# Kernel tuning notes

Hardware: AMD Instinct MI355X
Metric: run time of the kernel (lower is better)

The kernel has to match this reference:

```python
import jax, jax.numpy as jnp
import numpy as np

INPUT_DIM = 4096
BOTTLENECK = 32768
A = 2
K = 0.05
# eval-mode sparsity count: max(1, int(bottleneck * a * k))
K_COUNT = max(1, int(BOTTLENECK * A * K))  # 3276


def setup_inputs() -> dict:
    key = jax.random.key(0)
    kx, kw = jax.random.split(key)
    x = jax.random.normal(kx, (4096, INPUT_DIM), dtype=jnp.float32)
    # encoder weight [bottleneck, input_dim], like nn.Linear(input_dim, bottleneck)
    W = jax.random.normal(kw, (BOTTLENECK, INPUT_DIM), dtype=jnp.float32) * (1.0 / np.sqrt(INPUT_DIM))
    b_enc = jnp.zeros((BOTTLENECK,), dtype=jnp.float32)
    b_dec = jnp.zeros((INPUT_DIM,), dtype=jnp.float32)
    return {"x": x, "W": W, "b_enc": b_enc, "b_dec": b_dec, "epoch": 0}


def reference(x, W, b_enc, b_dec, epoch):
    # encode: z1 = x @ W^T + b_enc  -> [B, bottleneck]
    z1 = jnp.einsum("bi,hi->bh", x, W) + b_enc
    # eval-mode k-winner-take-all mask over dim 1
    _, topk_idx = jax.lax.top_k(z1, K_COUNT)  # [B, K_COUNT]
    rows = jnp.arange(z1.shape[0])[:, None]
    mask = jnp.zeros_like(z1).at[rows, topk_idx].set(1.0)
    a1 = z1 * mask
    # tied-weight decode: z2 = a1 @ W + b_dec -> [B, input_dim]
    z2 = jnp.einsum("bh,hi->bi", a1, W) + b_dec
    return z2
```

## Files before the change

kernel.cpp:

```cpp
#include <hip/hip_runtime.h>
#include <hip/hip_bf16.h>
#include <stdint.h>


#define DIM      4096
#define BATCH    4096
#define NROWS_W  32768
#define KCNT     3276
#define DELTA    0.0066f
#define ROWCAP   256
#define HCAP     64

typedef __bf16 bf16x8 __attribute__((ext_vector_type(8)));
typedef __bf16 bf16x4 __attribute__((ext_vector_type(4)));
typedef float  f32x4  __attribute__((ext_vector_type(4)));

__device__ __forceinline__ void gload_lds16(const void* g, void* l) {
  __builtin_amdgcn_global_load_lds(
      (const __attribute__((address_space(1))) void*)g,
      (__attribute__((address_space(3))) void*)l, 16, 0, 0);
}

__global__ void k_split(const float* __restrict__ s, __bf16* __restrict__ hi,
                        __bf16* __restrict__ lo, int n4) {
  int i = blockIdx.x * 256 + threadIdx.x;
  const int stride = gridDim.x * 256;
  for (; i < n4; i += stride) {
    f32x4 v = ((const f32x4*)s)[i];
    bf16x4 h, l;
#pragma unroll
    for (int j = 0; j < 4; ++j) {
      __bf16 hb = (__bf16)v[j];
      h[j] = hb;
      l[j] = (__bf16)(v[j] - (float)hb);
    }
    ((bf16x4*)hi)[i] = h;
    ((bf16x4*)lo)[i] = l;
  }
}

__global__ void k_splitw(const float* __restrict__ W, __bf16* __restrict__ Wh,
                         __bf16* __restrict__ Wt) {
  __shared__ __bf16 t[64][65];
  const int c0 = blockIdx.x * 64, r0 = blockIdx.y * 64;
  const int tx = threadIdx.x, ty = threadIdx.y;
  for (int rr = ty; rr < 64; rr += 8) {
    const float w = W[(long)(r0 + rr) * DIM + c0 + tx];
    const __bf16 h = (__bf16)w;
    Wh[(long)(r0 + rr) * DIM + c0 + tx] = h;
    t[rr][tx] = h;
  }
  __syncthreads();
  for (int cc = ty; cc < 64; cc += 8)
    Wt[(long)(c0 + cc) * NROWS_W + r0 + tx] = t[tx][cc];
}

__global__ __launch_bounds__(256, 2)
void k_gemm(const __bf16* __restrict__ A, const __bf16* __restrict__ B,
            const float* __restrict__ bias, float* __restrict__ C,
            int M, int N, int Kt) {
  constexpr int BM = 128, BN = 128, BK = 64;
  __shared__ __align__(16) __bf16 sA[BM * BK];
  __shared__ __align__(16) __bf16 sB[BN * BK];

  const int tid = threadIdx.x;
  const int nbn = N / BN;
  int bm, bn;
  if ((M / BM) % 16 == 0 && nbn % 32 == 0) {
    const int nsbn = nbn / 32;
    const int g = blockIdx.x >> 9, r = blockIdx.x & 511;
    bm = (g / nsbn) * 16 + (r >> 5);
    bn = (g % nsbn) * 32 + (r & 31);
  } else {
    bm = blockIdx.x / nbn;
    bn = blockIdx.x % nbn;
  }
  const int m0 = bm * BM, n0 = bn * BN;
  const int lane = tid & 63, wid = tid >> 6;
  const int wm = wid >> 1, wn = wid & 1;
  const int lr = lane & 15, lk = lane >> 4;
  const int swz = (lr & 7) << 4;

  f32x4 acc[4][4] = {};

  for (int k0 = 0; k0 < Kt; k0 += BK) {
#pragma unroll
    for (int r = 0; r < 4; ++r) {
      const int o = (r * 256 + tid) * 16;
      const int row = o >> 7;
      const int colb = (o & 127) ^ ((row & 7) << 4);
      const long gA = ((long)(m0 + row) * Kt + k0) * 2 + colb;
      const long gB = ((long)(n0 + row) * Kt + k0) * 2 + colb;
      gload_lds16((const char*)A + gA, (char*)sA + o);
      gload_lds16((const char*)B + gB, (char*)sB + o);
    }
    __syncthreads();

#pragma unroll
    for (int kk = 0; kk < 2; ++kk) {
      bf16x8 va[4], vb[4];
      const int kbase = (kk * 64 + lk * 16) ^ swz;
#pragma unroll
      for (int m = 0; m < 4; ++m) {
        const int row = wm * 64 + m * 16 + lr;
        va[m] = *(const bf16x8*)((const char*)sA + row * 128 + kbase);
      }
#pragma unroll
      for (int n = 0; n < 4; ++n) {
        const int row = wn * 64 + n * 16 + lr;
        vb[n] = *(const bf16x8*)((const char*)sB + row * 128 + kbase);
      }
#pragma unroll
      for (int m = 0; m < 4; ++m)
#pragma unroll
        for (int n = 0; n < 4; ++n)
          acc[m][n] = __builtin_amdgcn_mfma_f32_16x16x32_bf16(va[m], vb[n], acc[m][n], 0, 0, 0);
    }
    __syncthreads();
  }

#pragma unroll
  for (int n = 0; n < 4; ++n) {
    const int col = n0 + wn * 64 + n * 16 + lr;
    const float bv = bias[col];
#pragma unroll
    for (int m = 0; m < 4; ++m) {
      const int r0r = m0 + wm * 64 + m * 16 + lk * 4;
#pragma unroll
      for (int j = 0; j < 4; ++j)
        C[(long)(r0r + j) * N + col] = acc[m][n][j] + bv;
    }
  }
}

__device__ __forceinline__ unsigned f2o(float f) {
  unsigned b = __float_as_uint(f);
  return ((int)b < 0) ? ~b : (b | 0x80000000u);
}
__device__ __forceinline__ float o2f(unsigned u) {
  unsigned b = (u & 0x80000000u) ? (u & 0x7FFFFFFFu) : ~u;
  return __uint_as_float(b);
}

__global__ __launch_bounds__(256)
void k_topk3(const float* __restrict__ z1, float* __restrict__ thr,
             unsigned* __restrict__ rowlist, unsigned* __restrict__ rowcnt,
             unsigned* __restrict__ c1, unsigned* __restrict__ bucket,
             unsigned* __restrict__ bcnt, int kwant) {
  __shared__ unsigned hist[4096];
  __shared__ unsigned cand[3584];
  __shared__ unsigned s_n, s_bin, s_rem, s_wt[4], s_cnt, s_above;
  const int tid = threadIdx.x;
  const int b = blockIdx.x;
  const f32x4* zv = (const f32x4*)(z1 + (long)b * NROWS_W);
  constexpr int NV = NROWS_W / 4;

#pragma unroll
  for (int j = 0; j < 16; ++j) hist[tid + j * 256] = 0;
  if (tid == 0) { s_n = 0; s_cnt = 0; s_above = 0; }
  __syncthreads();
  for (int i = tid; i < NV; i += 256) {
    f32x4 v = zv[i];
#pragma unroll
    for (int j = 0; j < 4; ++j) atomicAdd(&hist[f2o(v[j]) >> 20], 1u);
  }
  __syncthreads();
  unsigned p = 0;
#pragma unroll
  for (int j = 0; j < 16; ++j) p += hist[tid * 16 + j];
  unsigned sfx = p;
  const int lane = tid & 63, w = tid >> 6;
#pragma unroll
  for (int off = 1; off < 64; off <<= 1) {
    unsigned o = __shfl_down(sfx, off);
    sfx += (lane + off < 64) ? o : 0u;
  }
  if (lane == 0) s_wt[w] = sfx;
  __syncthreads();
  unsigned above_waves = 0;
  for (int ww = w + 1; ww < 4; ++ww) above_waves += s_wt[ww];
  const unsigned incl = sfx + above_waves;
  const int cnt = __syncthreads_count(incl >= (unsigned)kwant);
  const int tstar = cnt - 1;
  if (tid == tstar) {
    unsigned cum = incl - p;
    int bsel = tid * 16;
    for (int j = 15; j >= 0; --j) {
      const unsigned h = hist[tid * 16 + j];
      if (cum + h >= (unsigned)kwant) { bsel = tid * 16 + j; break; }
      cum += h;
    }
    s_bin = (unsigned)bsel;
    s_rem = (unsigned)kwant - cum;
  }
  __syncthreads();
  const unsigned binsel = s_bin;
  unsigned rem = s_rem;

  for (int i = tid; i < NV; i += 256) {
    f32x4 v = zv[i];
#pragma unroll
    for (int j = 0; j < 4; ++j) {
      const unsigned u = f2o(v[j]);
      if ((u >> 20) == binsel) {
        const unsigned jj = atomicAdd(&s_n, 1u);
        if (jj < 3584u) cand[jj] = u & 0xFFFFFu;
      }
    }
  }
  __syncthreads();
  const int n = (s_n < 3584u) ? (int)s_n : 3584;
  unsigned pfx = 0;
#pragma unroll
  for (int pass = 0; pass < 3; ++pass) {
    const int shift = (pass == 0) ? 12 : (pass == 1) ? 4 : 0;
    const int nb = (pass == 2) ? 16 : 256;
    if (tid < 256) hist[tid] = 0;
    __syncthreads();
    for (int i = tid; i < n; i += 256) {
      const unsigned v = cand[i];
      const bool m = (pass == 0) ? true
                     : (pass == 1) ? ((v >> 12) == (pfx >> 12))
                                   : ((v >> 4) == (pfx >> 4));
      if (m) atomicAdd(&hist[(v >> shift) & (nb - 1)], 1u);
    }
    __syncthreads();
    if (tid == 0) {
      unsigned cum = 0;
      int d = nb - 1;
      for (; d > 0; --d) {
        if (cum + hist[d] >= rem) break;
        cum += hist[d];
      }
      s_bin = (unsigned)d;
      s_rem = rem - cum;
    }
    __syncthreads();
    pfx |= (s_bin << shift);
    rem = s_rem;
    __syncthreads();
  }
  const float t = o2f((binsel << 20) | pfx);
  if (tid == 0) thr[b] = t;
  __syncthreads();

  const float hi = t + DELTA, lo = t - DELTA;
  unsigned my_above = 0;
  for (int i = tid; i < NV; i += 256) {
    f32x4 v = zv[i];
#pragma unroll
    for (int j = 0; j < 4; ++j) {
      const float vv = v[j];
      my_above += (vv > hi) ? 1u : 0u;
      if (vv >= lo && vv <= hi) {
        const unsigned idx = (unsigned)(i * 4 + j);
        const unsigned jj = atomicAdd(&s_cnt, 1u);
        if (jj < ROWCAP) {
          rowlist[(long)b * ROWCAP + jj] = idx;
          const unsigned pq = atomicAdd(&bcnt[idx], 1u);
          if (pq < HCAP) bucket[(long)idx * HCAP + pq] = ((unsigned)b << 9) | jj;
        }
      }
    }
  }
  atomicAdd(&s_above, my_above);
  __syncthreads();
  if (tid == 0) {
    rowcnt[b] = (s_cnt < ROWCAP) ? s_cnt : ROWCAP;
    c1[b] = s_above;
  }
}

__global__ void k_zero(f32x4* __restrict__ p, int nvec) {
  int i = blockIdx.x * 256 + threadIdx.x;
  const int stride = gridDim.x * 256;
  f32x4 z = {0.f, 0.f, 0.f, 0.f};
  for (; i < nvec; i += stride) p[i] = z;
}

__global__ void k_recompute(const float* __restrict__ W, const __bf16* __restrict__ xh,
                            const __bf16* __restrict__ xl,
                            const unsigned* __restrict__ bucket,
                            const unsigned* __restrict__ bcnt,
                            float* __restrict__ exact) {
  const int h = blockIdx.x;
  unsigned n = bcnt[h];
  if (n > HCAP) n = HCAP;
  if (n == 0) return;
  __shared__ float wrec[DIM];
  const long wb = (long)h * DIM;
  for (int i = threadIdx.x; i < DIM / 4; i += 256)
    ((f32x4*)wrec)[i] = ((const f32x4*)(W + wb))[i];
  __syncthreads();
  const int w = threadIdx.x >> 6, lane = threadIdx.x & 63;
  for (unsigned e = w; e < n; e += 4) {
    const unsigned ent = bucket[(long)h * HCAP + e];
    const int b = ent >> 9, j = ent & 511;
    const bf16x8* ph = (const bf16x8*)(xh + (long)b * DIM);
    const bf16x8* pl = (const bf16x8*)(xl + (long)b * DIM);
    float s = 0.f;
#pragma unroll
    for (int c = 0; c < 8; ++c) {
      const int i8 = c * 64 + lane;
      bf16x8 vh = ph[i8], vl = pl[i8];
      const float* wr = &wrec[i8 * 8];
#pragma unroll
      for (int q = 0; q < 8; ++q) s += ((float)vh[q] + (float)vl[q]) * wr[q];
    }
#pragma unroll
    for (int m = 32; m; m >>= 1) s += __shfl_xor(s, m);
    if (lane == 0) exact[(long)b * ROWCAP + j] = s;
  }
}

__global__ void k_select(const float* __restrict__ exact, const unsigned* __restrict__ rowlist,
                         const unsigned* __restrict__ rowcnt, const unsigned* __restrict__ c1,
                         unsigned* __restrict__ bitmap) {
  const int b = blockIdx.x;
  const int n = (int)rowcnt[b];
  const int need = KCNT - (int)c1[b];
  __shared__ float vals[ROWCAP];
  const int j = threadIdx.x;
  vals[j] = (j < n) ? exact[(long)b * ROWCAP + j] : -1e30f;
  __syncthreads();
  if (j < n) {
    const float vj = vals[j];
    int rank = 0;
    for (int i = 0; i < n; ++i) {
      const float vi = vals[i];
      rank += (vi > vj || (vi == vj && i < j)) ? 1 : 0;
    }
    if (rank < need) {
      const unsigned h = rowlist[(long)b * ROWCAP + j];
      atomicOr(&bitmap[b * (NROWS_W / 32) + (h >> 5)], 1u << (h & 31));
    }
  }
}

__global__ void k_mask(const float* __restrict__ z1, const float* __restrict__ thr,
                       const unsigned* __restrict__ bitmap, __bf16* __restrict__ a1,
                       int n4, int ncols4) {
  int i = blockIdx.x * 256 + threadIdx.x;
  const int stride = gridDim.x * 256;
  for (; i < n4; i += stride) {
    f32x4 v = ((const f32x4*)z1)[i];
    const int row = i / ncols4;
    const int h0 = (i - row * ncols4) * 4;
    const float t = thr[row];
    const float hi = t + DELTA, lo = t - DELTA;
    const unsigned wbits = bitmap[row * (NROWS_W / 32) + (h0 >> 5)];
    bf16x4 o;
#pragma unroll
    for (int j = 0; j < 4; ++j) {
      const float vv = v[j];
      const bool sel = (vv > hi) || (vv >= lo && ((wbits >> ((h0 + j) & 31)) & 1u));
      o[j] = sel ? (__bf16)vv : (__bf16)0.0f;
    }
    ((bf16x4*)a1)[i] = o;
  }
}

extern "C" void kernel_launch(void* const* d_in, const int* in_sizes, int n_in,
                              void* d_out, int out_size, void* d_ws, size_t ws_size,
                              hipStream_t stream) {
  const float* x     = (const float*)d_in[0];
  const float* W     = (const float*)d_in[1];
  const float* b_enc = (const float*)d_in[2];
  const float* b_dec = (const float*)d_in[3];
  float* out = (float*)d_out;

  const long NW = (long)NROWS_W * DIM;
  const long NX = (long)BATCH * DIM;
  const long NZ = (long)BATCH * NROWS_W;

  char* ws = (char*)d_ws;
  __bf16* Wh = (__bf16*)ws;
  __bf16* Wt = Wh + NW;
  __bf16* xh = Wt + NW;
  __bf16* xl = xh + NX;
  float*  z1 = (float*)(xl + NX);
  float*  thr = z1 + NZ;
  char*   sc = (char*)(thr + BATCH);
  unsigned* rowcnt  = (unsigned*)sc;
  unsigned* c1      = (unsigned*)(sc + 16384);
  unsigned* bcnt    = (unsigned*)(sc + 32768);
  unsigned* bitmap  = (unsigned*)(sc + 163840);
  float*    exact   = (float*)(sc + 16941056);
  unsigned* rowlist = (unsigned*)(sc + 21135360);
  unsigned* bucket  = (unsigned*)(sc + 25329664);
  const long ZERO_OFF = 32768, ZERO_BYTES = 21069824;
  __bf16* a1 = Wh;

  const size_t needed = (size_t)(6 * NW + 4 * NX) + (size_t)4 * NZ + 4 * BATCH;
  if (ws_size < needed) return;

  k_splitw<<<dim3(DIM / 64, NROWS_W / 64), dim3(64, 8), 0, stream>>>(W, Wh, Wt);
  k_split<<<2048, 256, 0, stream>>>(x, xh, xl, (int)(NX / 4));

  k_gemm<<<(BATCH / 128) * (NROWS_W / 128), 256, 0, stream>>>(
      xh, Wh, b_enc, z1, BATCH, NROWS_W, DIM);

  k_zero<<<1024, 256, 0, stream>>>((f32x4*)(sc + ZERO_OFF), (int)(ZERO_BYTES / 16));
  k_topk3<<<BATCH, 256, 0, stream>>>(z1, thr, rowlist, rowcnt, c1, bucket, bcnt, KCNT);
  k_recompute<<<NROWS_W, 256, 0, stream>>>(W, xh, xl, bucket, bcnt, exact);
  k_select<<<BATCH, ROWCAP, 0, stream>>>(exact, rowlist, rowcnt, c1, bitmap);
  k_mask<<<2048, 256, 0, stream>>>(z1, thr, bitmap, a1, (int)(NZ / 4), NROWS_W / 4);

  k_gemm<<<(BATCH / 128) * (DIM / 128), 256, 0, stream>>>(
      a1, Wt, b_dec, out, BATCH, DIM, NROWS_W);
}
```

Baseline: 3.635 ms.

## Fuse mask into top-k, gather band candidates in LDS, drop x lo split

Result: faster. 3.553 ms (-2.3%).

```diff
diff --git a/kernel.cpp b/kernel.cpp
--- a/kernel.cpp
+++ b/kernel.cpp
@@ -10,6 +10,7 @@
 #define DELTA    0.0066f
 #define ROWCAP   256
 #define HCAP     64
+#define CANDCAP  3584
 
 typedef __bf16 bf16x8 __attribute__((ext_vector_type(8)));
 typedef __bf16 bf16x4 __attribute__((ext_vector_type(4)));
@@ -21,21 +22,15 @@
       (__attribute__((address_space(3))) void*)l, 16, 0, 0);
 }
 
-__global__ void k_split(const float* __restrict__ s, __bf16* __restrict__ hi,
-                        __bf16* __restrict__ lo, int n4) {
+__global__ void k_cvtx(const float* __restrict__ s, __bf16* __restrict__ hi, int n4) {
   int i = blockIdx.x * 256 + threadIdx.x;
   const int stride = gridDim.x * 256;
   for (; i < n4; i += stride) {
     f32x4 v = ((const f32x4*)s)[i];
-    bf16x4 h, l;
-#pragma unroll
-    for (int j = 0; j < 4; ++j) {
-      __bf16 hb = (__bf16)v[j];
-      h[j] = hb;
-      l[j] = (__bf16)(v[j] - (float)hb);
-    }
+    bf16x4 h;
+#pragma unroll
+    for (int j = 0; j < 4; ++j) h[j] = (__bf16)v[j];
     ((bf16x4*)hi)[i] = h;
-    ((bf16x4*)lo)[i] = l;
   }
 }
 
@@ -143,12 +138,13 @@
 }
 
 __global__ __launch_bounds__(256)
-void k_topk3(const float* __restrict__ z1, float* __restrict__ thr,
+void k_topk4(const float* __restrict__ z1, float* __restrict__ thr,
              unsigned* __restrict__ rowlist, unsigned* __restrict__ rowcnt,
              unsigned* __restrict__ c1, unsigned* __restrict__ bucket,
-             unsigned* __restrict__ bcnt, int kwant) {
+             unsigned* __restrict__ bcnt, __bf16* __restrict__ a1, int kwant) {
   __shared__ unsigned hist[4096];
-  __shared__ unsigned cand[3584];
+  __shared__ float cv[CANDCAP];
+  __shared__ unsigned short ci[CANDCAP];
   __shared__ unsigned s_n, s_bin, s_rem, s_wt[4], s_cnt, s_above;
   const int tid = threadIdx.x;
   const int b = blockIdx.x;
@@ -197,19 +193,22 @@
   const unsigned binsel = s_bin;
   unsigned rem = s_rem;
 
+  const unsigned blo = (binsel > 0) ? binsel - 1 : 0;
+  const unsigned bhi = (binsel < 4095) ? binsel + 1 : 4095;
   for (int i = tid; i < NV; i += 256) {
     f32x4 v = zv[i];
 #pragma unroll
     for (int j = 0; j < 4; ++j) {
-      const unsigned u = f2o(v[j]);
-      if ((u >> 20) == binsel) {
+      const unsigned bin = f2o(v[j]) >> 20;
+      if (bin >= blo && bin <= bhi) {
         const unsigned jj = atomicAdd(&s_n, 1u);
-        if (jj < 3584u) cand[jj] = u & 0xFFFFFu;
-      }
-    }
-  }
-  __syncthreads();
-  const int n = (s_n < 3584u) ? (int)s_n : 3584;
+        if (jj < CANDCAP) { cv[jj] = v[j]; ci[jj] = (unsigned short)(i * 4 + j); }
+      }
+    }
+  }
+  __syncthreads();
+  const int n = (s_n < CANDCAP) ? (int)s_n : CANDCAP;
+
   unsigned pfx = 0;
 #pragma unroll
   for (int pass = 0; pass < 3; ++pass) {
@@ -218,7 +217,9 @@
     if (tid < 256) hist[tid] = 0;
     __syncthreads();
     for (int i = tid; i < n; i += 256) {
-      const unsigned v = cand[i];
+      const unsigned u = f2o(cv[i]);
+      if ((u >> 20) != binsel) continue;
+      const unsigned v = u & 0xFFFFFu;
       const bool m = (pass == 0) ? true
                      : (pass == 1) ? ((v >> 12) == (pfx >> 12))
                                    : ((v >> 4) == (pfx >> 4));
@@ -242,26 +243,33 @@
   }
   const float t = o2f((binsel << 20) | pfx);
   if (tid == 0) thr[b] = t;
-  __syncthreads();
-
   const float hi = t + DELTA, lo = t - DELTA;
+
+  for (int i = tid; i < n; i += 256) {
+    const float v = cv[i];
+    if (v >= lo && v <= hi) {
+      const unsigned idx = ci[i];
+      const unsigned jj = atomicAdd(&s_cnt, 1u);
+      if (jj < ROWCAP) {
+        rowlist[(long)b * ROWCAP + jj] = idx;
+        const unsigned pq = atomicAdd(&bcnt[idx], 1u);
+        if (pq < HCAP) bucket[(long)idx * HCAP + pq] = ((unsigned)b << 9) | jj;
+      }
+    }
+  }
+
   unsigned my_above = 0;
+  bf16x4* av = (bf16x4*)(a1 + (long)b * NROWS_W);
   for (int i = tid; i < NV; i += 256) {
     f32x4 v = zv[i];
+    bf16x4 o;
 #pragma unroll
     for (int j = 0; j < 4; ++j) {
-      const float vv = v[j];
-      my_above += (vv > hi) ? 1u : 0u;
-      if (vv >= lo && vv <= hi) {
-        const unsigned idx = (unsigned)(i * 4 + j);
-        const unsigned jj = atomicAdd(&s_cnt, 1u);
-        if (jj < ROWCAP) {
-          rowlist[(long)b * ROWCAP + jj] = idx;
-          const unsigned pq = atomicAdd(&bcnt[idx], 1u);
-          if (pq < HCAP) bucket[(long)idx * HCAP + pq] = ((unsigned)b << 9) | jj;
-        }
-      }
-    }
+      const bool in = v[j] > hi;
+      my_above += in ? 1u : 0u;
+      o[j] = in ? (__bf16)v[j] : (__bf16)0.0f;
+    }
+    av[i] = o;
   }
   atomicAdd(&s_above, my_above);
   __syncthreads();
@@ -273,13 +281,13 @@
 
 __global__ void k_zero(f32x4* __restrict__ p, int nvec) {
   int i = blockIdx.x * 256 + threadIdx.x;
-  const int stride = gridDim.x * 256;
-  f32x4 z = {0.f, 0.f, 0.f, 0.f};
-  for (; i < nvec; i += stride) p[i] = z;
-}
-
-__global__ void k_recompute(const float* __restrict__ W, const __bf16* __restrict__ xh,
-                            const __bf16* __restrict__ xl,
+  if (i < nvec) {
+    f32x4 z = {0.f, 0.f, 0.f, 0.f};
+    p[i] = z;
+  }
+}
+
+__global__ void k_recompute(const float* __restrict__ W, const float* __restrict__ x,
                             const unsigned* __restrict__ bucket,
                             const unsigned* __restrict__ bcnt,
                             float* __restrict__ exact) {
@@ -296,16 +304,15 @@
   for (unsigned e = w; e < n; e += 4) {
     const unsigned ent = bucket[(long)h * HCAP + e];
     const int b = ent >> 9, j = ent & 511;
-    const bf16x8* ph = (const bf16x8*)(xh + (long)b * DIM);
-    const bf16x8* pl = (const bf16x8*)(xl + (long)b * DIM);
+    const f32x4* xv = (const f32x4*)(x + (long)b * DIM);
     float s = 0.f;
 #pragma unroll
-    for (int c = 0; c < 8; ++c) {
-      const int i8 = c * 64 + lane;
-      bf16x8 vh = ph[i8], vl = pl[i8];
-      const float* wr = &wrec[i8 * 8];
-#pragma unroll
-      for (int q = 0; q < 8; ++q) s += ((float)vh[q] + (float)vl[q]) * wr[q];
+    for (int c = 0; c < 16; ++c) {
+      const int i4 = c * 64 + lane;
+      f32x4 v = xv[i4];
+      const float* wr = &wrec[i4 * 4];
+#pragma unroll
+      for (int q = 0; q < 4; ++q) s += v[q] * wr[q];
     }
 #pragma unroll
     for (int m = 32; m; m >>= 1) s += __shfl_xor(s, m);
@@ -315,7 +322,7 @@
 
 __global__ void k_select(const float* __restrict__ exact, const unsigned* __restrict__ rowlist,
                          const unsigned* __restrict__ rowcnt, const unsigned* __restrict__ c1,
-                         unsigned* __restrict__ bitmap) {
+                         const float* __restrict__ z1, __bf16* __restrict__ a1) {
   const int b = blockIdx.x;
   const int n = (int)rowcnt[b];
   const int need = KCNT - (int)c1[b];
@@ -332,31 +339,9 @@
     }
     if (rank < need) {
       const unsigned h = rowlist[(long)b * ROWCAP + j];
-      atomicOr(&bitmap[b * (NROWS_W / 32) + (h >> 5)], 1u << (h & 31));
-    }
-  }
-}
-
-__global__ void k_mask(const float* __restrict__ z1, const float* __restrict__ thr,
-                       const unsigned* __restrict__ bitmap, __bf16* __restrict__ a1,
-                       int n4, int ncols4) {
-  int i = blockIdx.x * 256 + threadIdx.x;
-  const int stride = gridDim.x * 256;
-  for (; i < n4; i += stride) {
-    f32x4 v = ((const f32x4*)z1)[i];
-    const int row = i / ncols4;
-    const int h0 = (i - row * ncols4) * 4;
-    const float t = thr[row];
-    const float hi = t + DELTA, lo = t - DELTA;
-    const unsigned wbits = bitmap[row * (NROWS_W / 32) + (h0 >> 5)];
-    bf16x4 o;
-#pragma unroll
-    for (int j = 0; j < 4; ++j) {
-      const float vv = v[j];
-      const bool sel = (vv > hi) || (vv >= lo && ((wbits >> ((h0 + j) & 31)) & 1u));
-      o[j] = sel ? (__bf16)vv : (__bf16)0.0f;
-    }
-    ((bf16x4*)a1)[i] = o;
+      const long off = (long)b * NROWS_W + h;
+      a1[off] = (__bf16)z1[off];
+    }
   }
 }
 
@@ -377,34 +362,30 @@
   __bf16* Wh = (__bf16*)ws;
   __bf16* Wt = Wh + NW;
   __bf16* xh = Wt + NW;
-  __bf16* xl = xh + NX;
-  float*  z1 = (float*)(xl + NX);
+  float*  z1 = (float*)(xh + NX);
   float*  thr = z1 + NZ;
   char*   sc = (char*)(thr + BATCH);
   unsigned* rowcnt  = (unsigned*)sc;
   unsigned* c1      = (unsigned*)(sc + 16384);
   unsigned* bcnt    = (unsigned*)(sc + 32768);
-  unsigned* bitmap  = (unsigned*)(sc + 163840);
-  float*    exact   = (float*)(sc + 16941056);
-  unsigned* rowlist = (unsigned*)(sc + 21135360);
-  unsigned* bucket  = (unsigned*)(sc + 25329664);
-  const long ZERO_OFF = 32768, ZERO_BYTES = 21069824;
+  float*    exact   = (float*)(sc + 163840);
+  unsigned* rowlist = (unsigned*)(sc + 4358144);
+  unsigned* bucket  = (unsigned*)(sc + 8552448);
   __bf16* a1 = Wh;
 
-  const size_t needed = (size_t)(6 * NW + 4 * NX) + (size_t)4 * NZ + 4 * BATCH;
+  const size_t needed = (size_t)(4 * NW + 2 * NX) + (size_t)4 * NZ + 4 * BATCH + 17000000;
   if (ws_size < needed) return;
 
   k_splitw<<<dim3(DIM / 64, NROWS_W / 64), dim3(64, 8), 0, stream>>>(W, Wh, Wt);
-  k_split<<<2048, 256, 0, stream>>>(x, xh, xl, (int)(NX / 4));
+  k_cvtx<<<2048, 256, 0, stream>>>(x, xh, (int)(NX / 4));
 
   k_gemm<<<(BATCH / 128) * (NROWS_W / 128), 256, 0, stream>>>(
       xh, Wh, b_enc, z1, BATCH, NROWS_W, DIM);
 
-  k_zero<<<1024, 256, 0, stream>>>((f32x4*)(sc + ZERO_OFF), (int)(ZERO_BYTES / 16));
-  k_topk3<<<BATCH, 256, 0, stream>>>(z1, thr, rowlist, rowcnt, c1, bucket, bcnt, KCNT);
-  k_recompute<<<NROWS_W, 256, 0, stream>>>(W, xh, xl, bucket, bcnt, exact);
-  k_select<<<BATCH, ROWCAP, 0, stream>>>(exact, rowlist, rowcnt, c1, bitmap);
-  k_mask<<<2048, 256, 0, stream>>>(z1, thr, bitmap, a1, (int)(NZ / 4), NROWS_W / 4);
+  k_zero<<<32, 256, 0, stream>>>((f32x4*)bcnt, 131072 / 16);
+  k_topk4<<<BATCH, 256, 0, stream>>>(z1, thr, rowlist, rowcnt, c1, bucket, bcnt, a1, KCNT);
+  k_recompute<<<NROWS_W, 256, 0, stream>>>(W, x, bucket, bcnt, exact);
+  k_select<<<BATCH, ROWCAP, 0, stream>>>(exact, rowlist, rowcnt, c1, z1, a1);
 
   k_gemm<<<(BATCH / 128) * (DIM / 128), 256, 0, stream>>>(
       a1, Wt, b_dec, out, BATCH, DIM, NROWS_W);
```
